# Performance work log

Measured on AMD Instinct MI355X. Metric: run time of the kernel, lower is better.

The kernel has to match this reference:

```python
import jax, jax.numpy as jnp
import numpy as np

N_EDGES = 4096   # num_edges n
D = 2            # stalk_dim
FEAT = 128       # edge_feature_dim
H0 = 64          # hidden_dims[0]
H1 = 64          # hidden_dims[1]
MLP_H = 64       # SheafBuilder MLP hidden
CLS_H = 128      # classifier mlp_hidden_dim
NCLS = 8         # num_classes
OFFS = np.array([-4, -3, -2, -1, 1, 2, 3, 4])  # symmetric ring, degree 8


def setup_inputs() -> dict:
    key = jax.random.key(0)
    ks = jax.random.split(key, 10)
    n, deg = N_EDGES, len(OFFS)
    # directed adjacency pairs (i, j) of the edge-to-edge graph (from L1 nonzeros)
    i = np.repeat(np.arange(n), deg)
    t = np.tile(np.arange(deg), n)
    j = (i + OFFS[t]) % n
    rev = j * deg + (deg - 1 - t)  # index of the reverse pair (j, i)

    def gn(k, shape, scale):
        return jax.random.normal(k, shape, jnp.float32) * scale

    return {
        "edge_features": gn(ks[0], (n, FEAT), 1.0),
        # input_embedding
        "We": gn(ks[1], (FEAT, H0), 0.08), "be": jnp.zeros((H0,), jnp.float32),
        # SheafBuilder MLP: Linear(2F,64) -> ReLU -> Linear(64, d)
        "M1w": gn(ks[2], (2 * FEAT, MLP_H), 0.06), "M1b": jnp.zeros((MLP_H,), jnp.float32),
        "M2w": gn(ks[3], (MLP_H, D), 0.12), "M2b": jnp.zeros((D,), jnp.float32),
        # SCN layer
        "W1": gn(ks[4], (D, D), 0.5),
        "W2": gn(ks[5], (H0, H1), 0.12),
        # classifier MLP
        "Wc1": gn(ks[6], (H1, CLS_H), 0.1), "bc1": jnp.zeros((CLS_H,), jnp.float32),
        "Wc2": gn(ks[7], (CLS_H, NCLS), 0.1), "bc2": jnp.zeros((NCLS,), jnp.float32),
        # constant graph structure (replaces L1 nonzero pattern)
        "adj_i": jnp.asarray(i, jnp.int32),
        "adj_j": jnp.asarray(j, jnp.int32),
        "rev_idx": jnp.asarray(rev, jnp.int32),
    }


def _build_delta(edge_features, M1w, M1b, M2w, M2b, adj_i, adj_j, rev_idx, n, d):
    """Diagonal-sheaf restriction maps + dense normalized sheaf Laplacian."""
    nd = n * d
    # SheafBuilder: per-pair diagonal restriction map params p_(i,j) in R^d
    pair = jnp.concatenate([edge_features[adj_i], edge_features[adj_j]], axis=1)  # (P, 2F)
    h = jax.nn.relu(pair @ M1w + M1b)
    p = h @ M2w + M2b                                                            # (P, d)
    # diagonal blocks: sum_{j} F_ij^T F_ij = diag(sum p^2) per source edge i
    s = jax.ops.segment_sum(p * p, adj_i, num_segments=n)                        # (n, d)
    # dense LF
    LF = jnp.zeros((nd, nd), jnp.float32)
    diag_idx = jnp.arange(nd)
    LF = LF.at[diag_idx, diag_idx].set(s.reshape(nd))
    ar = jnp.arange(d)
    rows = (adj_i[:, None] * d + ar).reshape(-1)
    cols = (adj_j[:, None] * d + ar).reshape(-1)
    offvals = (-(p[rev_idx] * p)).reshape(-1)  # block(v,u) = -F_uv^T F_vu (diagonal)
    LF = LF.at[rows, cols].set(offvals)
    # D^{-1/2}: diagonal blocks are diagonal -> eigh reduces to elementwise rsqrt
    dvals = s.reshape(nd) + 1e-5
    dinv = 1.0 / jnp.sqrt(jnp.clip(dvals, 1e-6))
    return dinv[:, None] * LF * dinv[None, :]  # Delta_F, (nd, nd)


def reference(edge_features, We, be, M1w, M1b, M2w, M2b, W1, W2, Wc1, bc1, Wc2, bc2,
              adj_i, adj_j, rev_idx):
    n = edge_features.shape[0]
    d = W1.shape[0]
    nd = n * d
    Delta = _build_delta(edge_features, M1w, M1b, M2w, M2b, adj_i, adj_j, rev_idx, n, d)
    # input embedding, broadcast over stalk dim
    H = jax.nn.relu(edge_features @ We + be)                     # (n, H0)
    X = jnp.broadcast_to(H[:, None, :], (n, d, H.shape[1]))      # (n, d, H0)
    # SCN layer: Y = elu((I - Delta)(I_n (x) W1^T) X W2)
    Xt = jnp.einsum('ba,nbc->nac', W1, X).reshape(nd, -1) @ W2   # (nd, H1)
    Y = jax.nn.elu(Xt - Delta @ Xt)                              # (nd, H1)
    # global mean pool + classifier (dropout inactive at inference)
    pooled = Y.mean(axis=0)                                      # (H1,)
    logits = jax.nn.relu(pooled @ Wc1 + bc1) @ Wc2 + bc2         # (NCLS,)
    return logits
```

## Files before the change

kernel.cpp:

```cpp
#include <hip/hip_runtime.h>
#include <hip/hip_bf16.h>


#define NN    4096
#define CHK   32
#define EXT   48
#define PEXT  40
#define NGRID 128
#define WS_R17 (NGRID * 64u * 4u)

#define NBLK2 256
#define PEXT2 24
#define WS_PIPE ((3u * NN * 64u + NBLK2 * 64u) * 4u)

struct Smem {
    float As[EXT][64];
    float Bs[EXT][64];
    float Gs[EXT][64];
    float Hs[16][64];
    float ps[PEXT][8][2];
    float dinvs[PEXT][2];
    float facs[PEXT][2];
    float red[1024];
    float pooled[64];
    float hid[128];
};

struct SmemK1 {
    float Wa[128][64];
    float Wb[128][64];
    float Wh[128][64];
    float W2s[64][64];
    float efs[16][128];
    float Hs[16][64];
};

struct SmemK2 {
    float As[PEXT2][64];
    float Bs[32][64];
    float Gs[32][64];
    float ps[PEXT2][8][2];
    float dinvs[PEXT2][2];
    float facs[PEXT2][2];
    float red[1024];
};

struct SmemFin {
    float Wc1s[64][128];
    float Wc2s[128][8];
    float red[256];
    float pooled[64];
    float hid[128];
};

template <bool F32>
static __device__ __forceinline__ float ldv(const void* p, int i) {
    if constexpr (F32) return ((const float*)p)[i];
    else return __bfloat162float(((const __hip_bfloat16*)p)[i]);
}

static __device__ __forceinline__ float ldr(const void* p, int i, bool f32) {
    if (f32) return ((const float*)p)[i];
    return __bfloat162float(((const __hip_bfloat16*)p)[i]);
}

static __device__ __forceinline__ float blo(unsigned u) {
    return __uint_as_float(u << 16);
}
static __device__ __forceinline__ float bhi(unsigned u) {
    return __uint_as_float(u & 0xFFFF0000u);
}

template <bool F32>
static __device__ void body(Smem& sm,
    const void* ef, const void* We, const void* be, const void* M1w,
    const void* M1b, const void* M2w, const void* M2b, const void* W1,
    const void* W2, const void* Wc1, const void* bc1, const void* Wc2,
    const void* bc2, void* out)
{
    const int t = threadIdx.x;
    const int c = t & 63;
    const int w = t >> 6;
    const int a = (t >> 6) & 1;
    const int ms = t >> 7;

    const float m1b_c = ldv<F32>(M1b, c);
    const float m2w0  = ldv<F32>(M2w, c * 2 + 0);
    const float m2w1  = ldv<F32>(M2w, c * 2 + 1);
    const float m2b0  = ldv<F32>(M2b, 0);
    const float m2b1  = ldv<F32>(M2b, 1);
    const float cs0 = ldv<F32>(W1, 0) + ldv<F32>(W1, 2);
    const float cs1 = ldv<F32>(W1, 1) + ldv<F32>(W1, 3);
    const float bec = ldv<F32>(be, c);

    float accY = 0.f;

    for (int ch = blockIdx.x; ch < NN / CHK; ch += gridDim.x) {
        const int c0 = ch * CHK;
        for (int pp = 0; pp < EXT / 16; ++pp) {
            const int q  = pp * 16 + w;
            const int gi = (c0 - 8 + q) & (NN - 1);
            float aA = 0.f, aB = 0.f, aH = bec;
            #pragma unroll 2
            for (int k = 0; k < 128; ++k) {
                const float ev = ldv<F32>(ef, gi * 128 + k);
                aA += ev * ldv<F32>(M1w, k * 64 + c);
                aB += ev * ldv<F32>(M1w, 8192 + k * 64 + c);
                aH += ev * ldv<F32>(We, k * 64 + c);
            }
            sm.As[q][c] = aA;
            sm.Bs[q][c] = aB;
            sm.Hs[w][c] = fmaxf(aH, 0.f);
            __syncthreads();
            float aG = 0.f;
            #pragma unroll 2
            for (int k = 0; k < 64; ++k)
                aG += sm.Hs[w][k] * ldv<F32>(W2, k * 64 + c);
            sm.Gs[q][c] = aG;
            __syncthreads();
        }
        for (int pi = w; pi < PEXT * 8; pi += 16) {
            const int r  = pi >> 3;
            const int tt = pi & 7;
            const int off = (tt < 4) ? (tt - 4) : (tt - 3);
            const float h = fmaxf(sm.As[r + 4][c] + sm.Bs[r + 4 + off][c] + m1b_c, 0.f);
            float q0 = h * m2w0, q1 = h * m2w1;
            #pragma unroll
            for (int d2 = 32; d2; d2 >>= 1) {
                q0 += __shfl_xor(q0, d2);
                q1 += __shfl_xor(q1, d2);
            }
            if (c == 0) {
                sm.ps[r][tt][0] = q0 + m2b0;
                sm.ps[r][tt][1] = q1 + m2b1;
            }
        }
        __syncthreads();
        if (t < PEXT * 2) {
            const int r = t >> 1, aa = t & 1;
            float s = 0.f;
            #pragma unroll
            for (int tt = 0; tt < 8; ++tt) { const float p = sm.ps[r][tt][aa]; s += p * p; }
            const float dv = 1.f / sqrtf(fmaxf(s + 1e-5f, 1e-6f));
            sm.dinvs[r][aa] = dv;
            sm.facs[r][aa]  = 1.f - dv * dv * s;
        }
        __syncthreads();
        const float csa = a ? cs1 : cs0;
        #pragma unroll
        for (int it = 0; it < 4; ++it) {
            const int m = it * 8 + ms;
            const int r = m + 4;
            const int g = m + 8;
            const float di = sm.dinvs[r][a];
            float v = sm.facs[r][a] * sm.Gs[g][c];
            #pragma unroll
            for (int tt = 0; tt < 8; ++tt) {
                const int off = (tt < 4) ? (tt - 4) : (tt - 3);
                v += di * sm.ps[r + off][7 - tt][a] * sm.ps[r][tt][a]
                        * sm.dinvs[r + off][a] * sm.Gs[g + off][c];
            }
            const float x = csa * v;
            accY += (x > 0.f) ? x : expm1f(x);
        }
        __syncthreads();
    }

    sm.red[t] = accY;
    __syncthreads();

    if (gridDim.x > 1) {
        if (t < 64) {
            float s = 0.f;
            #pragma unroll
            for (int g2 = 0; g2 < 16; ++g2) s += sm.red[(g2 << 6) + t];
            ((float*)out)[blockIdx.x * 64 + t] = s;
        }
        return;
    }

    if (t < 64) {
        float s = 0.f;
        #pragma unroll
        for (int g2 = 0; g2 < 16; ++g2) s += sm.red[(g2 << 6) + t];
        sm.pooled[t] = s * (1.f / 8192.f);
    }
    __syncthreads();
    if (t < 128) {
        float acc = ldv<F32>(bc1, t);
        #pragma unroll 8
        for (int k = 0; k < 64; ++k) acc += sm.pooled[k] * ldv<F32>(Wc1, k * 128 + t);
        sm.hid[t] = fmaxf(acc, 0.f);
    }
    __syncthreads();
    if (t < 8) {
        float acc = ldv<F32>(bc2, t);
        #pragma unroll 8
        for (int k = 0; k < 128; ++k) acc += sm.hid[k] * ldv<F32>(Wc2, k * 8 + t);
        if constexpr (F32) ((float*)out)[t] = acc;
        else ((__hip_bfloat16*)out)[t] = __float2bfloat16(acc);
    }
}

template <bool F32>
static __device__ void k1body(SmemK1& sm,
    const void* ef, const void* We, const void* be, const void* M1w,
    const void* W2, float* A, float* B, float* G)
{
    const int t = threadIdx.x, c = t & 63, w = t >> 6;
    const int base = blockIdx.x * 16;

    if constexpr (F32) {
        for (int idx = t; idx < 128 * 64; idx += 1024) {
            const int k = idx >> 6, cc = idx & 63;
            sm.Wa[k][cc] = ((const float*)M1w)[idx];
            sm.Wb[k][cc] = ((const float*)M1w)[8192 + idx];
            sm.Wh[k][cc] = ((const float*)We)[idx];
        }
        for (int idx = t; idx < 64 * 64; idx += 1024)
            sm.W2s[idx >> 6][idx & 63] = ((const float*)W2)[idx];
        for (int idx = t; idx < 16 * 128; idx += 1024)
            sm.efs[idx >> 7][idx & 127] = ((const float*)ef)[(base << 7) + idx];
    } else {
        for (int j = t; j < 4096; j += 1024) {
            const int k = j >> 5, c2 = (j & 31) * 2;
            const unsigned a = ((const unsigned*)M1w)[j];
            sm.Wa[k][c2] = blo(a);  sm.Wa[k][c2 + 1] = bhi(a);
            const unsigned b = ((const unsigned*)M1w)[4096 + j];
            sm.Wb[k][c2] = blo(b);  sm.Wb[k][c2 + 1] = bhi(b);
            const unsigned h = ((const unsigned*)We)[j];
            sm.Wh[k][c2] = blo(h);  sm.Wh[k][c2 + 1] = bhi(h);
        }
        for (int j = t; j < 2048; j += 1024) {
            const int k = j >> 5, c2 = (j & 31) * 2;
            const unsigned v = ((const unsigned*)W2)[j];
            sm.W2s[k][c2] = blo(v);  sm.W2s[k][c2 + 1] = bhi(v);
        }
        for (int j = t; j < 16 * 64; j += 1024) {
            const int n = j >> 6, kk = (j & 63) * 2;
            const unsigned u = ((const unsigned*)ef)[(base << 6) + j];
            sm.efs[n][kk] = blo(u);  sm.efs[n][kk + 1] = bhi(u);
        }
    }
    __syncthreads();

    const int n = w;
    float aA = 0.f, aB = 0.f, aH = ldv<F32>(be, c);
    #pragma unroll 8
    for (int k = 0; k < 128; ++k) {
        const float e = sm.efs[n][k];
        aA = fmaf(e, sm.Wa[k][c], aA);
        aB = fmaf(e, sm.Wb[k][c], aB);
        aH = fmaf(e, sm.Wh[k][c], aH);
    }
    A[((base + n) << 6) + c] = aA;
    B[((base + n) << 6) + c] = aB;
    sm.Hs[n][c] = fmaxf(aH, 0.f);
    __syncthreads();

    float aG = 0.f;
    #pragma unroll 8
    for (int k = 0; k < 64; ++k)
        aG = fmaf(sm.Hs[n][k], sm.W2s[k][c], aG);
    G[((base + n) << 6) + c] = aG;
}

__global__ __launch_bounds__(1024) void sheaf_k1(
    const void* ef, const void* We, const void* be, const void* M1w,
    const void* W2, float* A, float* B, float* G)
{
    __shared__ SmemK1 sm;
    __shared__ int flag;
    const int t = threadIdx.x;
    if (t == 0) flag = 0;
    __syncthreads();
    {
        const __hip_bfloat16* efh = (const __hip_bfloat16*)ef;
        bool big = false;
        #pragma unroll
        for (int k = 0; k < 8; ++k) {
            const float v = __bfloat162float(efh[t * 8 + k]);
            big |= !(fabsf(v) < 1e4f);
        }
        if (big) atomicOr(&flag, 1);
    }
    __syncthreads();
    if (flag) k1body<true >(sm, ef, We, be, M1w, W2, A, B, G);
    else      k1body<false>(sm, ef, We, be, M1w, W2, A, B, G);
}

template <bool F32>
static __device__ void k2body(SmemK2& sm,
    const void* M1b, const void* M2w, const void* M2b, const void* W1,
    const float* A, const float* B, const float* G, float* partials)
{
    const int t = threadIdx.x, c = t & 63, w = t >> 6;
    const int base = blockIdx.x * 16;

    for (int idx = t; idx < PEXT2 * 64; idx += 1024) {
        const int r = idx >> 6, cc = idx & 63;
        sm.As[r][cc] = A[(((base - 4 + r) & (NN - 1)) << 6) + cc];
    }
    for (int idx = t; idx < 32 * 64; idx += 1024) {
        const int r = idx >> 6, cc = idx & 63;
        const int gi = ((base - 8 + r) & (NN - 1)) << 6;
        sm.Bs[r][cc] = B[gi + cc];
        sm.Gs[r][cc] = G[gi + cc];
    }
    __syncthreads();

    const float m1b_c = ldv<F32>(M1b, c);
    const float m2w0  = ldv<F32>(M2w, c * 2 + 0);
    const float m2w1  = ldv<F32>(M2w, c * 2 + 1);
    const float m2b0  = ldv<F32>(M2b, 0);
    const float m2b1  = ldv<F32>(M2b, 1);
    const float cs0 = ldv<F32>(W1, 0) + ldv<F32>(W1, 2);
    const float cs1 = ldv<F32>(W1, 1) + ldv<F32>(W1, 3);

    for (int pi = w; pi < PEXT2 * 8; pi += 16) {
        const int r  = pi >> 3;
        const int tt = pi & 7;
        const int off = (tt < 4) ? (tt - 4) : (tt - 3);
        const float h = fmaxf(sm.As[r][c] + sm.Bs[r + 4 + off][c] + m1b_c, 0.f);
        float q0 = h * m2w0, q1 = h * m2w1;
        #pragma unroll
        for (int d2 = 32; d2; d2 >>= 1) {
            q0 += __shfl_xor(q0, d2);
            q1 += __shfl_xor(q1, d2);
        }
        if (c == 0) {
            sm.ps[r][tt][0] = q0 + m2b0;
            sm.ps[r][tt][1] = q1 + m2b1;
        }
    }
    __syncthreads();

    if (t < PEXT2 * 2) {
        const int r = t >> 1, aa = t & 1;
        float s = 0.f;
        #pragma unroll
        for (int tt = 0; tt < 8; ++tt) { const float p = sm.ps[r][tt][aa]; s += p * p; }
        const float dv = 1.f / sqrtf(fmaxf(s + 1e-5f, 1e-6f));
        sm.dinvs[r][aa] = dv;
        sm.facs[r][aa]  = 1.f - dv * dv * s;
    }
    __syncthreads();

    float accY = 0.f;
    #pragma unroll
    for (int it = 0; it < 2; ++it) {
        const int m = it * 8 + (t >> 7);
        const int a = (t >> 6) & 1;
        const int r = m + 4;
        const int g = m + 8;
        const float csa = a ? cs1 : cs0;
        const float di = sm.dinvs[r][a];
        float v = sm.facs[r][a] * sm.Gs[g][c];
        #pragma unroll
        for (int tt = 0; tt < 8; ++tt) {
            const int off = (tt < 4) ? (tt - 4) : (tt - 3);
            v += di * sm.ps[r + off][7 - tt][a] * sm.ps[r][tt][a]
                    * sm.dinvs[r + off][a] * sm.Gs[g + off][c];
        }
        const float x = csa * v;
        accY += (x > 0.f) ? x : expm1f(x);
    }

    sm.red[t] = accY;
    __syncthreads();
    if (t < 64) {
        float s = 0.f;
        #pragma unroll
        for (int g2 = 0; g2 < 16; ++g2) s += sm.red[(g2 << 6) + t];
        partials[blockIdx.x * 64 + t] = s;
    }
}

__global__ __launch_bounds__(1024) void sheaf_k2(
    const void* ef, const void* M1b, const void* M2w, const void* M2b,
    const void* W1, const float* A, const float* B, const float* G,
    float* partials)
{
    __shared__ SmemK2 sm;
    __shared__ int flag;
    const int t = threadIdx.x;
    if (t == 0) flag = 0;
    __syncthreads();
    {
        const __hip_bfloat16* efh = (const __hip_bfloat16*)ef;
        bool big = false;
        #pragma unroll
        for (int k = 0; k < 8; ++k) {
            const float v = __bfloat162float(efh[t * 8 + k]);
            big |= !(fabsf(v) < 1e4f);
        }
        if (big) atomicOr(&flag, 1);
    }
    __syncthreads();
    if (flag) k2body<true >(sm, M1b, M2w, M2b, W1, A, B, G, partials);
    else      k2body<false>(sm, M1b, M2w, M2b, W1, A, B, G, partials);
}

template <bool F32>
static __device__ void finbody(SmemFin& sm,
    const void* Wc1, const void* bc1, const void* Wc2, const void* bc2,
    const float* partials, int nparts, void* out)
{
    const int t = threadIdx.x;

    if constexpr (F32) {
        for (int idx = t; idx < 64 * 128; idx += 256)
            sm.Wc1s[idx >> 7][idx & 127] = ((const float*)Wc1)[idx];
        for (int idx = t; idx < 128 * 8; idx += 256)
            sm.Wc2s[idx >> 3][idx & 7] = ((const float*)Wc2)[idx];
    } else {
        for (int j = t; j < 4096; j += 256) {
            const int k = j >> 6, c2 = (j & 63) * 2;
            const unsigned u = ((const unsigned*)Wc1)[j];
            sm.Wc1s[k][c2] = blo(u);  sm.Wc1s[k][c2 + 1] = bhi(u);
        }
        for (int j = t; j < 512; j += 256) {
            const int k = j >> 2, c2 = (j & 3) * 2;
            const unsigned u = ((const unsigned*)Wc2)[j];
            sm.Wc2s[k][c2] = blo(u);  sm.Wc2s[k][c2 + 1] = bhi(u);
        }
    }

    const int h = t & 63, g = t >> 6;
    float s = 0.f;
    for (int b = g; b < nparts; b += 4) s += partials[b * 64 + h];
    sm.red[t] = s;
    __syncthreads();
    if (t < 64)
        sm.pooled[t] = (sm.red[t] + sm.red[t + 64] + sm.red[t + 128] + sm.red[t + 192])
                       * (1.f / 8192.f);
    __syncthreads();
    if (t < 128) {
        float acc = ldv<F32>(bc1, t);
        #pragma unroll 8
        for (int k = 0; k < 64; ++k) acc = fmaf(sm.pooled[k], sm.Wc1s[k][t], acc);
        sm.hid[t] = fmaxf(acc, 0.f);
    }
    __syncthreads();
    if (t < 8) {
        float acc = ldv<F32>(bc2, t);
        #pragma unroll 8
        for (int k = 0; k < 128; ++k) acc = fmaf(sm.hid[k], sm.Wc2s[k][t], acc);
        if constexpr (F32) ((float*)out)[t] = acc;
        else ((__hip_bfloat16*)out)[t] = __float2bfloat16(acc);
    }
}

__global__ __launch_bounds__(256) void sheaf_finalize(
    const void* ef, const void* Wc1, const void* bc1, const void* Wc2,
    const void* bc2, const float* partials, int nparts, void* out)
{
    __shared__ SmemFin sm;
    __shared__ int flag;
    const int t = threadIdx.x;
    if (t == 0) flag = 0;
    __syncthreads();
    {
        const __hip_bfloat16* efh = (const __hip_bfloat16*)ef;
        bool big = false;
        #pragma unroll
        for (int k = 0; k < 8; ++k) {
            const float v = __bfloat162float(efh[t * 8 + k]);
            big |= !(fabsf(v) < 1e4f);
        }
        if (big) atomicOr(&flag, 1);
    }
    __syncthreads();
    if (flag) finbody<true >(sm, Wc1, bc1, Wc2, bc2, partials, nparts, out);
    else      finbody<false>(sm, Wc1, bc1, Wc2, bc2, partials, nparts, out);
}

__global__ __launch_bounds__(1024) void SheafConvolutionalNetwork_81698867905240_kernel(
    const void* ef, const void* We, const void* be, const void* M1w,
    const void* M1b, const void* M2w, const void* M2b, const void* W1,
    const void* W2, const void* Wc1, const void* bc1, const void* Wc2,
    const void* bc2, void* out)
{
    __shared__ Smem sm;
    __shared__ int flag;
    const int t = threadIdx.x;
    if (t == 0) flag = 0;
    __syncthreads();
    {
        const __hip_bfloat16* efh = (const __hip_bfloat16*)ef;
        bool big = false;
        #pragma unroll
        for (int k = 0; k < 8; ++k) {
            const float v = __bfloat162float(efh[t * 8 + k]);
            big |= !(fabsf(v) < 1e4f);
        }
        if (big) atomicOr(&flag, 1);
    }
    __syncthreads();
    if (flag)
        body<true >(sm, ef, We, be, M1w, M1b, M2w, M2b, W1, W2, Wc1, bc1, Wc2, bc2, out);
    else
        body<false>(sm, ef, We, be, M1w, M1b, M2w, M2b, W1, W2, Wc1, bc1, Wc2, bc2, out);
}

extern "C" void kernel_launch(void* const* d_in, const int* in_sizes, int n_in,
                              void* d_out, int out_size, void* d_ws, size_t ws_size,
                              hipStream_t stream)
{
    (void)in_sizes; (void)n_in; (void)out_size;
    (void)hipGetLastError();

    if (d_ws != nullptr && ws_size >= (size_t)WS_PIPE) {
        float* A = (float*)d_ws;
        float* B = A + NN * 64;
        float* G = B + NN * 64;
        float* partials = G + NN * 64;
        sheaf_k1<<<dim3(NBLK2), dim3(1024), 0, stream>>>(
            d_in[0], d_in[1], d_in[2], d_in[3], d_in[8], A, B, G);
        sheaf_k2<<<dim3(NBLK2), dim3(1024), 0, stream>>>(
            d_in[0], d_in[4], d_in[5], d_in[6], d_in[7], A, B, G, partials);
        sheaf_finalize<<<dim3(1), dim3(256), 0, stream>>>(
            d_in[0], d_in[9], d_in[10], d_in[11], d_in[12],
            partials, NBLK2, d_out);
    } else if (d_ws != nullptr && ws_size >= (size_t)WS_R17) {
        SheafConvolutionalNetwork_81698867905240_kernel<<<dim3(NGRID), dim3(1024), 0, stream>>>(
            d_in[0], d_in[1], d_in[2], d_in[3], d_in[4], d_in[5], d_in[6],
            d_in[7], d_in[8], d_in[9], d_in[10], d_in[11], d_in[12], d_ws);
        sheaf_finalize<<<dim3(1), dim3(256), 0, stream>>>(
            d_in[0], d_in[9], d_in[10], d_in[11], d_in[12],
            (const float*)d_ws, NGRID, d_out);
    } else {
        SheafConvolutionalNetwork_81698867905240_kernel<<<dim3(1), dim3(1024), 0, stream>>>(
            d_in[0], d_in[1], d_in[2], d_in[3], d_in[4], d_in[5], d_in[6],
            d_in[7], d_in[8], d_in[9], d_in[10], d_in[11], d_in[12], d_out);
    }

    if (hipGetLastError() != hipSuccess)
        (void)hipMemsetAsync(d_out, 0x41, 16, stream);
}
```

Before: 53.71 us.

## Rewrite first pipeline kernel with bf16 MFMA and compact bf16 shared weights

The first stage kernel now runs with 256 threads per block and computes the three 128-wide projections (A, B and the embedding H) with v_mfma_f32_16x16x32_bf16 inline assembly. The weights are kept as raw bf16 in a padded concatenated shared array rather than being expanded to fp32. The aim is to cut the shared-memory staging traffic and the scalar FMA work per block. The G projection uses a transposed bf16 W2 with four rows per thread. The fp32 fallback becomes a simple scalar loop, and manual s_nop hazard padding after the MFMAs adds some fragility.

```diff
diff --git a/kernel.cpp b/kernel.cpp
--- a/kernel.cpp
+++ b/kernel.cpp
@@ -12,6 +12,9 @@
 #define NBLK2 256
 #define PEXT2 24
 #define WS_PIPE ((3u * NN * 64u + NBLK2 * 64u) * 4u)
+
+typedef float v4f __attribute__((ext_vector_type(4)));
+typedef int   v4i __attribute__((ext_vector_type(4)));
 
 struct Smem {
     float As[EXT][64];
@@ -26,15 +29,6 @@
     float hid[128];
 };
 
-struct SmemK1 {
-    float Wa[128][64];
-    float Wb[128][64];
-    float Wh[128][64];
-    float W2s[64][64];
-    float efs[16][128];
-    float Hs[16][64];
-};
-
 struct SmemK2 {
     float As[PEXT2][64];
     float Bs[32][64];
@@ -202,74 +196,13 @@
     }
 }
 
-template <bool F32>
-static __device__ void k1body(SmemK1& sm,
+__global__ __launch_bounds__(256) void sheaf_k1(
     const void* ef, const void* We, const void* be, const void* M1w,
     const void* W2, float* A, float* B, float* G)
 {
-    const int t = threadIdx.x, c = t & 63, w = t >> 6;
-    const int base = blockIdx.x * 16;
-
-    if constexpr (F32) {
-        for (int idx = t; idx < 128 * 64; idx += 1024) {
-            const int k = idx >> 6, cc = idx & 63;
-            sm.Wa[k][cc] = ((const float*)M1w)[idx];
-            sm.Wb[k][cc] = ((const float*)M1w)[8192 + idx];
-            sm.Wh[k][cc] = ((const float*)We)[idx];
-        }
-        for (int idx = t; idx < 64 * 64; idx += 1024)
-            sm.W2s[idx >> 6][idx & 63] = ((const float*)W2)[idx];
-        for (int idx = t; idx < 16 * 128; idx += 1024)
-            sm.efs[idx >> 7][idx & 127] = ((const float*)ef)[(base << 7) + idx];
-    } else {
-        for (int j = t; j < 4096; j += 1024) {
-            const int k = j >> 5, c2 = (j & 31) * 2;
-            const unsigned a = ((const unsigned*)M1w)[j];
-            sm.Wa[k][c2] = blo(a);  sm.Wa[k][c2 + 1] = bhi(a);
-            const unsigned b = ((const unsigned*)M1w)[4096 + j];
-            sm.Wb[k][c2] = blo(b);  sm.Wb[k][c2 + 1] = bhi(b);
-            const unsigned h = ((const unsigned*)We)[j];
-            sm.Wh[k][c2] = blo(h);  sm.Wh[k][c2 + 1] = bhi(h);
-        }
-        for (int j = t; j < 2048; j += 1024) {
-            const int k = j >> 5, c2 = (j & 31) * 2;
-            const unsigned v = ((const unsigned*)W2)[j];
-            sm.W2s[k][c2] = blo(v);  sm.W2s[k][c2 + 1] = bhi(v);
-        }
-        for (int j = t; j < 16 * 64; j += 1024) {
-            const int n = j >> 6, kk = (j & 63) * 2;
-            const unsigned u = ((const unsigned*)ef)[(base << 6) + j];
-            sm.efs[n][kk] = blo(u);  sm.efs[n][kk + 1] = bhi(u);
-        }
-    }
-    __syncthreads();
-
-    const int n = w;
-    float aA = 0.f, aB = 0.f, aH = ldv<F32>(be, c);
-    #pragma unroll 8
-    for (int k = 0; k < 128; ++k) {
-        const float e = sm.efs[n][k];
-        aA = fmaf(e, sm.Wa[k][c], aA);
-        aB = fmaf(e, sm.Wb[k][c], aB);
-        aH = fmaf(e, sm.Wh[k][c], aH);
-    }
-    A[((base + n) << 6) + c] = aA;
-    B[((base + n) << 6) + c] = aB;
-    sm.Hs[n][c] = fmaxf(aH, 0.f);
-    __syncthreads();
-
-    float aG = 0.f;
-    #pragma unroll 8
-    for (int k = 0; k < 64; ++k)
-        aG = fmaf(sm.Hs[n][k], sm.W2s[k][c], aG);
-    G[((base + n) << 6) + c] = aG;
-}
-
-__global__ __launch_bounds__(1024) void sheaf_k1(
-    const void* ef, const void* We, const void* be, const void* M1w,
-    const void* W2, float* A, float* B, float* G)
-{
-    __shared__ SmemK1 sm;
+    __shared__ unsigned short Wcat[128][194];
+    __shared__ unsigned short W2T[64][66];
+    __shared__ float Hs[16][64];
     __shared__ int flag;
     const int t = threadIdx.x;
     if (t == 0) flag = 0;
@@ -285,8 +218,127 @@
         if (big) atomicOr(&flag, 1);
     }
     __syncthreads();
-    if (flag) k1body<true >(sm, ef, We, be, M1w, W2, A, B, G);
-    else      k1body<false>(sm, ef, We, be, M1w, W2, A, B, G);
+    const int nb = blockIdx.x * 16;
+
+    if (!flag) {
+        unsigned* Wc32 = (unsigned*)&Wcat[0][0];
+        const unsigned* M1u = (const unsigned*)M1w;
+        const unsigned* Weu = (const unsigned*)We;
+        #pragma unroll
+        for (int rep = 0; rep < 16; ++rep) {
+            const int s = rep * 256 + t;
+            const int k = s >> 5, jj = s & 31;
+            Wc32[k * 97 + jj]      = M1u[s];
+            Wc32[k * 97 + 32 + jj] = M1u[4096 + s];
+            Wc32[k * 97 + 64 + jj] = Weu[s];
+        }
+        const unsigned short* W2h = (const unsigned short*)W2;
+        #pragma unroll
+        for (int rep = 0; rep < 16; ++rep) {
+            const int s = rep * 256 + t;
+            W2T[s & 63][s >> 6] = W2h[s];
+        }
+        __syncthreads();
+
+        const int l = t & 63, w = t >> 6;
+        const int grp = l >> 4, c16 = l & 15;
+        const int nt0 = w * 3;
+        v4f acc0 = {0.f, 0.f, 0.f, 0.f}, acc1 = acc0, acc2 = acc0;
+        const unsigned short* efu = (const unsigned short*)ef;
+        #pragma unroll
+        for (int ks = 0; ks < 4; ++ks) {
+            const v4i av = *(const v4i*)(efu + (nb + c16) * 128 + ks * 32 + grp * 8);
+            #pragma unroll
+            for (int q = 0; q < 3; ++q) {
+                const int nt = nt0 + q;
+                const unsigned short* src = &Wcat[ks * 32 + grp * 8][nt * 16 + c16];
+                v4i bv;
+                unsigned short* bu = (unsigned short*)&bv;
+                #pragma unroll
+                for (int jj = 0; jj < 8; ++jj) bu[jj] = src[jj * 194];
+                if (q == 0)
+                    asm volatile("v_mfma_f32_16x16x32_bf16 %0, %1, %2, %0"
+                                 : "+v"(acc0) : "v"(av), "v"(bv));
+                else if (q == 1)
+                    asm volatile("v_mfma_f32_16x16x32_bf16 %0, %1, %2, %0"
+                                 : "+v"(acc1) : "v"(av), "v"(bv));
+                else
+                    asm volatile("v_mfma_f32_16x16x32_bf16 %0, %1, %2, %0"
+                                 : "+v"(acc2) : "v"(av), "v"(bv));
+            }
+        }
+        asm volatile("s_nop 7\n\ts_nop 7");
+
+        #pragma unroll
+        for (int q = 0; q < 3; ++q) {
+            const int nt = nt0 + q;
+            const v4f accv = (q == 0) ? acc0 : (q == 1) ? acc1 : acc2;
+            #pragma unroll
+            for (int r = 0; r < 4; ++r) {
+                const int node = nb + grp * 4 + r;
+                const float v = accv[r];
+                if (nt < 4) {
+                    A[node * 64 + nt * 16 + c16] = v;
+                } else if (nt < 8) {
+                    B[node * 64 + (nt - 4) * 16 + c16] = v;
+                } else {
+                    const float bec = __bfloat162float(
+                        ((const __hip_bfloat16*)be)[(nt - 8) * 16 + c16]);
+                    Hs[grp * 4 + r][(nt - 8) * 16 + c16] = fmaxf(v + bec, 0.f);
+                }
+            }
+        }
+        __syncthreads();
+
+        {
+            const int c = t & 63;
+            const unsigned* W2T32 = (const unsigned*)&W2T[0][0];
+            float g0 = 0.f, g1 = 0.f, g2 = 0.f, g3 = 0.f;
+            #pragma unroll 4
+            for (int kk = 0; kk < 32; ++kk) {
+                const unsigned wv = W2T32[c * 33 + kk];
+                const float w0 = blo(wv), w1 = bhi(wv);
+                const float2 h0 = *(const float2*)&Hs[4 * w + 0][2 * kk];
+                const float2 h1 = *(const float2*)&Hs[4 * w + 1][2 * kk];
+                const float2 h2 = *(const float2*)&Hs[4 * w + 2][2 * kk];
+                const float2 h3 = *(const float2*)&Hs[4 * w + 3][2 * kk];
+                g0 += h0.x * w0 + h0.y * w1;
+                g1 += h1.x * w0 + h1.y * w1;
+                g2 += h2.x * w0 + h2.y * w1;
+                g3 += h3.x * w0 + h3.y * w1;
+            }
+            G[(nb + 4 * w + 0) * 64 + c] = g0;
+            G[(nb + 4 * w + 1) * 64 + c] = g1;
+            G[(nb + 4 * w + 2) * 64 + c] = g2;
+            G[(nb + 4 * w + 3) * 64 + c] = g3;
+        }
+    } else {
+        const float* eff = (const float*)ef;
+        const float* M1f = (const float*)M1w;
+        const float* Wef = (const float*)We;
+        for (int o = t; o < 16 * 192; o += 256) {
+            const int n = o / 192, j = o % 192;
+            float s = (j >= 128) ? ((const float*)be)[j - 128] : 0.f;
+            for (int k = 0; k < 128; ++k) {
+                const float e = eff[(nb + n) * 128 + k];
+                const float wv = (j < 64) ? M1f[k * 64 + j]
+                               : (j < 128) ? M1f[8192 + k * 64 + (j - 64)]
+                               : Wef[k * 64 + (j - 128)];
+                s += e * wv;
+            }
+            if (j < 64) A[(nb + n) * 64 + j] = s;
+            else if (j < 128) B[(nb + n) * 64 + (j - 64)] = s;
+            else Hs[n][j - 128] = fmaxf(s, 0.f);
+        }
+        __syncthreads();
+        const float* W2f = (const float*)W2;
+        for (int o = t; o < 16 * 64; o += 256) {
+            const int n = o >> 6, c = o & 63;
+            float s = 0.f;
+            for (int k = 0; k < 64; ++k) s += Hs[n][k] * W2f[k * 64 + c];
+            G[(nb + n) * 64 + c] = s;
+        }
+    }
 }
 
 template <bool F32>
@@ -515,7 +567,7 @@
         float* B = A + NN * 64;
         float* G = B + NN * 64;
         float* partials = G + NN * 64;
-        sheaf_k1<<<dim3(NBLK2), dim3(1024), 0, stream>>>(
+        sheaf_k1<<<dim3(NBLK2), dim3(256), 0, stream>>>(
             d_in[0], d_in[1], d_in[2], d_in[3], d_in[8], A, B, G);
         sheaf_k2<<<dim3(NBLK2), dim3(1024), 0, stream>>>(
             d_in[0], d_in[4], d_in[5], d_in[6], d_in[7], A, B, G, partials);
```

Result: slower. 141.9 us (+164.3%).
